# Kernel optimization log

Measured on AMD Instinct MI355X. Metric: run time of the kernel, lower is better.

## Reference

```python
import jax, jax.numpy as jnp
from jax import lax
import numpy as np

# Model hyper-parameters (from init_kwargs)
B = 4
POINT_NUM = 32768
SKP_NUM = 512
ISK_NUM = 2
K1 = 32                       # skp_neighbor_num
K2 = int(K1 * SKP_NUM * 4 / POINT_NUM)   # = 2, as computed in __init__
RADIUS_SCALING = 1.5
SPHERE_N = 128                # points per sphere template


def _fibonacci_sphere(n):
    i = np.arange(n, dtype=np.float64) + 0.5
    phi = np.arccos(1.0 - 2.0 * i / n)
    theta = np.pi * (1.0 + 5.0 ** 0.5) * i
    return np.stack([np.cos(theta) * np.sin(phi),
                     np.sin(theta) * np.sin(phi),
                     np.cos(phi)], axis=-1).astype(np.float32)


def setup_inputs() -> dict:
    key = jax.random.key(0)
    xyz = jax.random.normal(key, (B, POINT_NUM, 3), dtype=jnp.float32)
    sphere_template = jnp.asarray(_fibonacci_sphere(SPHERE_N))  # [S,3] unit sphere
    return {"xyz": xyz, "sphere_template": sphere_template}


def _fps(xyz, n):
    """Iterative furthest point sampling. xyz: [B,N,3] -> indices [B,n] int32."""
    b, N, _ = xyz.shape
    dist0 = jnp.full((b, N), 1e10, dtype=xyz.dtype)
    last0 = jnp.zeros((b,), dtype=jnp.int32)

    def step(carry, _):
        dist, last = carry
        lp = jnp.take_along_axis(xyz, last[:, None, None], axis=1)  # [B,1,3]
        d = jnp.sum((xyz - lp) ** 2, axis=-1)                        # [B,N]
        dist = jnp.minimum(dist, d)
        nxt = jnp.argmax(dist, axis=-1).astype(jnp.int32)
        return (dist, nxt), last

    (_, _), idxs = lax.scan(step, (dist0, last0), None, length=n)
    return idxs.T  # [B,n]


def _pairwise_sqdist(centers, pts):
    # [B,M,N] squared distances
    c2 = jnp.sum(centers ** 2, axis=-1)[:, :, None]
    p2 = jnp.sum(pts ** 2, axis=-1)[:, None, :]
    cp = jnp.einsum('bmd,bnd->bmn', centers, pts)
    return c2 + p2 - 2.0 * cp


def _sklnz(centers, pts, k):
    """SkeletonizationBlock: move each center to the mean of its k nearest
    points in pts; radius = mean distance to those neighbors."""
    d2 = _pairwise_sqdist(centers, pts)          # [B,M,N]
    neg, idx = lax.top_k(-d2, k)                 # [B,M,k]
    nb = jax.vmap(lambda x, i: x[i])(pts, idx)   # [B,M,k,3]
    new_centers = jnp.mean(nb, axis=2)
    radius = jnp.mean(jnp.sqrt(jnp.clip(-neg, 0.0)), axis=2)  # [B,M]
    return new_centers, radius


def _forward(xyz, sphere_template):
    # Stage 1: FPS to 4*skp_num seeds, then iterative skeletonization
    ids = _fps(xyz, SKP_NUM * 4)                               # [B,4*skp]
    centers = jnp.take_along_axis(xyz, ids[:, :, None], axis=1)
    radius = None
    for _ in range(ISK_NUM):
        centers, radius = _sklnz(centers, xyz, K1)
    # Stage 2: FPS on intermediate skeleton down to skp_num
    xyz2 = centers
    ids2 = _fps(xyz2, SKP_NUM)                                 # [B,skp]
    centers = jnp.take_along_axis(xyz2, ids2[:, :, None], axis=1)
    radius = jnp.take_along_axis(radius, ids2, axis=1)
    for _ in range(ISK_NUM):
        centers, _radius = _sklnz(centers, xyz2, K2)
    radius = (radius + _radius) * RADIUS_SCALING               # [B,skp]
    # Sphere reconstruction: template scaled by radius, translated to centers
    sphere_points = centers[:, :, None, :] + radius[:, :, None, None] * sphere_template[None, None]
    return centers, sphere_points, radius


def reference(xyz, sphere_template):
    return _forward(xyz, sphere_template)
```

## Files before the change

kernel.cpp:

```cpp
#include <hip/hip_runtime.h>
#include <cstdint>

#define BATCH 4
#define NPTS  32768
#define QN    8192
#define SKP   512
#define M1    (SKP*4)
#define KA    32
#define KB    2
#define SPHN  128

__device__ __forceinline__ float sqdist(float px, float py, float pz,
                                        float cx, float cy, float cz) {
  float dx = px - cx, dy = py - cy, dz = pz - cz;
  return __fadd_rn(__fadd_rn(__fmul_rn(dx, dx), __fmul_rn(dy, dy)),
                   __fmul_rn(dz, dz));
}
__device__ __forceinline__ float d2gram(float px, float py, float pz,
                                        float qx, float qy, float qz, float q2) {
  float p2 = __fadd_rn(__fadd_rn(__fmul_rn(px, px), __fmul_rn(py, py)),
                       __fmul_rn(pz, pz));
  float cp = __fadd_rn(__fadd_rn(__fmul_rn(qx, px), __fmul_rn(qy, py)),
                       __fmul_rn(qz, pz));
  return __fsub_rn(__fadd_rn(q2, p2), __fadd_rn(cp, cp));
}

__device__ __forceinline__ unsigned long long shfl_xor_u64(unsigned long long v, int off) {
  int lo = __shfl_xor((int)(unsigned)v, off);
  int hi = __shfl_xor((int)(unsigned)(v >> 32), off);
  return ((unsigned long long)(unsigned)hi << 32) | (unsigned)lo;
}
__device__ __forceinline__ unsigned long long shfl_u64(unsigned long long v, int src) {
  int lo = __shfl((int)(unsigned)v, src);
  int hi = __shfl((int)(unsigned)(v >> 32), src);
  return ((unsigned long long)(unsigned)hi << 32) | (unsigned)lo;
}

__global__ __launch_bounds__(1024)
void fps1_kernel(const float* __restrict__ xyz, int* __restrict__ ids,
                 unsigned long long* __restrict__ sync)
{
  int blk = blockIdx.x;
  int b = blk >> 2, sub = blk & 3;
  const float* X = xyz + (size_t)b * NPTS * 3;
  ids += (size_t)b * M1;
  int tid = threadIdx.x, lane = tid & 63, wave = tid >> 6;
  int base = sub * QN;

  __shared__ float2 xysh[QN];
  __shared__ unsigned long long s_w[16][2];
  __shared__ float s_pivc[16][3];
  __shared__ int s_J;

  float zr[8], dist[8];
#pragma unroll
  for (int j = 0; j < 8; ++j) {
    int pl = tid + 1024 * j;
    int pg = base + pl;
    xysh[pl] = make_float2(X[3*pg], X[3*pg+1]);
    zr[j] = X[3*pg+2];
    dist[j] = 1e10f;
  }
  if (tid == 0) {
    s_pivc[0][0] = X[0]; s_pivc[0][1] = X[1]; s_pivc[0][2] = X[2];
    if (sub == 0) ids[0] = 0;
  }
  __syncthreads();

  int it = 1, J = 1, rc = 1;

  while (it < M1) {
    for (int jp0 = 0; jp0 < J; jp0 += 4) {
      float pxa[4], pya[4], pza[4];
#pragma unroll
      for (int l = 0; l < 4; ++l) {
        int jj = jp0 + l; jj = (jj < J) ? jj : jp0;
        pxa[l] = s_pivc[jj][0]; pya[l] = s_pivc[jj][1]; pza[l] = s_pivc[jj][2];
      }
#pragma unroll
      for (int j = 0; j < 8; ++j) {
        int pl = tid + 1024 * j;
        float2 c2 = xysh[pl];
        float dd = dist[j];
#pragma unroll
        for (int l = 0; l < 4; ++l)
          dd = fminf(dd, sqdist(c2.x, c2.y, zr[j], pxa[l], pya[l], pza[l]));
        dist[j] = dd;
      }
    }
    unsigned long long k1 = 0, k2 = 0;
#pragma unroll
    for (int j = 0; j < 8; ++j) {
      int pg = base + tid + 1024 * j;
      unsigned long long key =
          ((unsigned long long)__float_as_uint(dist[j]) << 15) |
          (unsigned)(0x7FFF - pg);
      if (key > k1) { k2 = k1; k1 = key; }
      else if (key > k2) { k2 = key; }
    }
#pragma unroll
    for (int off = 32; off > 0; off >>= 1) {
      unsigned long long o1 = shfl_xor_u64(k1, off);
      unsigned long long o2 = shfl_xor_u64(k2, off);
      if (o1 > k1) { unsigned long long t = k1; k1 = o1; k2 = (t > o2) ? t : o2; }
      else         { k2 = (k2 > o1) ? k2 : o1; }
    }
    if (lane == 0) { s_w[wave][0] = k1; s_w[wave][1] = k2; }
    __syncthreads();
    if (wave == 0) {
      unsigned long long c1 = 0, c2v = 0;
      if (lane < 16) { c1 = s_w[lane][0]; c2v = s_w[lane][1]; }
      unsigned long long fb = c2v;
#pragma unroll
      for (int off = 8; off > 0; off >>= 1) {
        unsigned long long o = shfl_xor_u64(fb, off);
        if (o > fb) fb = o;
      }
      fb = shfl_u64(fb, 0);
      unsigned tag = (unsigned)rc;
      int par = rc & 1;
      int sbase = ((b * 2 + par) * 4 + sub) * 20;
      if (lane < 16)
        __hip_atomic_store(&sync[sbase + lane], (c1 << 12) | tag,
                           __ATOMIC_RELAXED, __HIP_MEMORY_SCOPE_AGENT);
      if (lane == 0)
        __hip_atomic_store(&sync[sbase + 16], (fb << 12) | tag,
                           __ATOMIC_RELAXED, __HIP_MEMORY_SCOPE_AGENT);
      unsigned long long ck = c1;
      unsigned long long rfk = 0;
      int cslot = 0, fslot = 0;
      bool needc = (lane >= 16), needf = (lane >= 1 && lane <= 3);
      if (needc) {
        int rsub = (sub + (lane >> 4)) & 3;
        cslot = ((b * 2 + par) * 4 + rsub) * 20 + (lane & 15);
      }
      if (needf) {
        int rsub = (sub + lane) & 3;
        fslot = ((b * 2 + par) * 4 + rsub) * 20 + 16;
      }
      while (__any(needc || needf)) {
        if (needc) {
          unsigned long long v = __hip_atomic_load(&sync[cslot],
                                  __ATOMIC_RELAXED, __HIP_MEMORY_SCOPE_AGENT);
          if ((unsigned)(v & 0xFFFu) == tag) { ck = v >> 12; needc = false; }
        }
        if (needf) {
          unsigned long long v = __hip_atomic_load(&sync[fslot],
                                  __ATOMIC_RELAXED, __HIP_MEMORY_SCOPE_AGENT);
          if ((unsigned)(v & 0xFFFu) == tag) { rfk = v >> 12; needf = false; }
        }
      }
      unsigned long long f = fb;
      unsigned long long f1 = shfl_u64(rfk, 1);
      unsigned long long f2 = shfl_u64(rfk, 2);
      unsigned long long f3 = shfl_u64(rfk, 3);
      if (f1 > f) f = f1;
      if (f2 > f) f = f2;
      if (f3 > f) f = f3;
      int ci = 0x7FFF - (int)(ck & 0x7FFFu);
      float cx = X[3*ci], cy = X[3*ci+1], cz = X[3*ci+2];
      int Jn = 0;
      while (it + Jn < M1 && Jn < 16) {
        unsigned long long mk = ck;
#pragma unroll
        for (int off = 32; off > 0; off >>= 1) {
          unsigned long long o = shfl_xor_u64(mk, off);
          if (o > mk) mk = o;
        }
        if (!(mk > f)) break;
        unsigned long long ball = __ballot(ck == mk);
        int wl = __ffsll(ball) - 1;
        float px = __shfl(cx, wl), py = __shfl(cy, wl), pz = __shfl(cz, wl);
        if (lane == 0) {
          s_pivc[Jn][0] = px; s_pivc[Jn][1] = py; s_pivc[Jn][2] = pz;
          if (sub == 0) ids[it + Jn] = 0x7FFF - (int)(mk & 0x7FFFu);
        }
        float d = sqdist(cx, cy, cz, px, py, pz);
        float nv = fminf(__uint_as_float((unsigned)(ck >> 15)), d);
        ck = ((unsigned long long)__float_as_uint(nv) << 15) | (ck & 0x7FFFu);
        ++Jn;
      }
      if (lane == 0) s_J = Jn;
    }
    __syncthreads();
    J = s_J;
    it += J;
    rc += 1;
  }
}

__global__ __launch_bounds__(256)
void fps2_kernel(const float4* __restrict__ pts, int* __restrict__ ids)
{
  const int PTS = 8, BLOCK = 256, NW = 4;
  int b = blockIdx.x;
  pts += (size_t)b * M1;
  ids += (size_t)b * SKP;
  int tid = threadIdx.x, lane = tid & 63, wave = tid >> 6;

  __shared__ float4 pl[M1];
  __shared__ float s_v[2][NW];
  __shared__ int   s_i[2][NW];

  float dist[PTS];
#pragma unroll
  for (int j = 0; j < PTS; ++j) {
    int p = tid + BLOCK * j;
    pl[p] = pts[p];
    dist[j] = 1e10f;
  }
  __syncthreads();

  if (tid == 0) ids[0] = 0;
  float4 piv = pl[0];
  float cx = piv.x, cy = piv.y, cz = piv.z;

  for (int it = 1; it < SKP; ++it) {
    float best = -1.f; int besti = 0;
#pragma unroll
    for (int j = 0; j < PTS; ++j) {
      int p = tid + BLOCK * j;
      float4 f = pl[p];
      float d = sqdist(f.x, f.y, f.z, cx, cy, cz);
      d = fminf(dist[j], d);
      dist[j] = d;
      bool gt = d > best;
      best  = gt ? d : best;
      besti = gt ? p : besti;
    }
#pragma unroll
    for (int off = 32; off > 0; off >>= 1) {
      float ov = __shfl_xor(best, off);
      int   oi = __shfl_xor(besti, off);
      if (ov > best || (ov == best && oi < besti)) { best = ov; besti = oi; }
    }
    int par = it & 1;
    if (lane == 0) { s_v[par][wave] = best; s_i[par][wave] = besti; }
    __syncthreads();
    float v = -1.f; int i = 0x7fffffff;
    if (lane < NW) { v = s_v[par][lane]; i = s_i[par][lane]; }
#pragma unroll
    for (int off = NW >> 1; off > 0; off >>= 1) {
      float ov = __shfl_xor(v, off);
      int   oi = __shfl_xor(i, off);
      if (ov > v || (ov == v && oi < i)) { v = ov; i = oi; }
    }
    i = __shfl(i, 0);
    if (tid == 0) ids[it] = i;
    float4 pv = pl[i];
    cx = pv.x; cy = pv.y; cz = pv.z;
  }
}

template<int K, int KL, int N, bool S3>
__global__ __launch_bounds__(256)
void sklnz_kernel(const float4* __restrict__ queries,
                  const void*   __restrict__ ptsv,
                  float4* __restrict__ outc,
                  float*  __restrict__ outr,
                  int M)
{
  const int CH = N / 64;
  int wave = threadIdx.x >> 6, lane = threadIdx.x & 63;
  int qid = blockIdx.x * 4 + wave;
  int b = qid / M;
  const float*  P3 = (const float*)ptsv + (size_t)b * N * 3;
  const float4* P4 = (const float4*)ptsv + (size_t)b * N;
  float4 q = queries[qid];
  float q2 = __fadd_rn(__fadd_rn(__fmul_rn(q.x, q.x), __fmul_rn(q.y, q.y)),
                       __fmul_rn(q.z, q.z));

  __shared__ float heads[4][64][K + 1];

  float a[KL];
#pragma unroll
  for (int s = 0; s < KL; ++s) a[s] = 3.0e38f;
  for (int j = 0; j < CH; ++j) {
    int p = lane + 64 * j;
    float px, py, pz;
    if (S3) { px = P3[3*p]; py = P3[3*p+1]; pz = P3[3*p+2]; }
    else    { float4 f = P4[p]; px = f.x; py = f.y; pz = f.z; }
    float d = d2gram(px, py, pz, q.x, q.y, q.z, q2);
#pragma unroll
    for (int s = KL - 1; s > 0; --s) a[s] = fminf(a[s], fmaxf(a[s-1], d));
    a[0] = fminf(a[0], d);
  }
#pragma unroll
  for (int s = 0; s < KL; ++s) heads[wave][lane][s] = a[s];
  heads[wave][lane][KL] = 3.1e38f;
  int h = 0; float t = 0.f;
  for (int r = 0; r < K; ++r) {
    float mv = heads[wave][lane][h];
    int   ml = lane;
#pragma unroll
    for (int off = 32; off > 0; off >>= 1) {
      float ov = __shfl_xor(mv, off);
      int   ol = __shfl_xor(ml, off);
      if (ov < mv || (ov == mv && ol < ml)) { mv = ov; ml = ol; }
    }
    t = mv;
    if (ml == lane) h++;
  }

  float sx = 0.f, sy = 0.f, sz = 0.f, sr = 0.f;
  int cl = 0;
  int myNext = 0x7fffffff;
  for (int j = 0; j < CH; ++j) {
    int p = lane + 64 * j;
    float px, py, pz;
    if (S3) { px = P3[3*p]; py = P3[3*p+1]; pz = P3[3*p+2]; }
    else    { float4 f = P4[p]; px = f.x; py = f.y; pz = f.z; }
    float d = d2gram(px, py, pz, q.x, q.y, q.z, q2);
    if (d < t) { sx += px; sy += py; sz += pz; sr += sqrtf(fmaxf(d, 0.f)); cl++; }
    else if (d == t && myNext == 0x7fffffff) myNext = p;
  }
  int ctot = cl;
#pragma unroll
  for (int off = 32; off > 0; off >>= 1) ctot += __shfl_xor(ctot, off);

  if constexpr (KL < K) {
    if (ctot >= K) {
      float a2[K];
#pragma unroll
      for (int s = 0; s < K; ++s) a2[s] = 3.0e38f;
      for (int j = 0; j < CH; ++j) {
        int p = lane + 64 * j;
        float px, py, pz;
        if (S3) { px = P3[3*p]; py = P3[3*p+1]; pz = P3[3*p+2]; }
        else    { float4 f = P4[p]; px = f.x; py = f.y; pz = f.z; }
        float d = d2gram(px, py, pz, q.x, q.y, q.z, q2);
#pragma unroll
        for (int s = K - 1; s > 0; --s) a2[s] = fminf(a2[s], fmaxf(a2[s-1], d));
        a2[0] = fminf(a2[0], d);
      }
#pragma unroll
      for (int s = 0; s < K; ++s) heads[wave][lane][s] = a2[s];
      heads[wave][lane][K] = 3.1e38f;
      h = 0;
      for (int r = 0; r < K; ++r) {
        float mv = heads[wave][lane][h];
        int   ml = lane;
#pragma unroll
        for (int off = 32; off > 0; off >>= 1) {
          float ov = __shfl_xor(mv, off);
          int   ol = __shfl_xor(ml, off);
          if (ov < mv || (ov == mv && ol < ml)) { mv = ov; ml = ol; }
        }
        t = mv;
        if (ml == lane) h++;
      }
      sx = sy = sz = sr = 0.f; cl = 0; myNext = 0x7fffffff;
      for (int j = 0; j < CH; ++j) {
        int p = lane + 64 * j;
        float px, py, pz;
        if (S3) { px = P3[3*p]; py = P3[3*p+1]; pz = P3[3*p+2]; }
        else    { float4 f = P4[p]; px = f.x; py = f.y; pz = f.z; }
        float d = d2gram(px, py, pz, q.x, q.y, q.z, q2);
        if (d < t) { sx += px; sy += py; sz += pz; sr += sqrtf(fmaxf(d, 0.f)); cl++; }
        else if (d == t && myNext == 0x7fffffff) myNext = p;
      }
      ctot = cl;
#pragma unroll
      for (int off = 32; off > 0; off >>= 1) ctot += __shfl_xor(ctot, off);
    }
  }

  int need = K - ctot;
  float rt = sqrtf(fmaxf(t, 0.f));

  for (int e = 0; e < need; ++e) {
    int mn = myNext;
#pragma unroll
    for (int off = 32; off > 0; off >>= 1) mn = min(mn, __shfl_xor(mn, off));
    if (myNext == mn) {
      float px, py, pz;
      if (S3) { px = P3[3*mn]; py = P3[3*mn+1]; pz = P3[3*mn+2]; }
      else    { float4 f = P4[mn]; px = f.x; py = f.y; pz = f.z; }
      sx += px; sy += py; sz += pz; sr += rt;
      int nx = 0x7fffffff;
      for (int j = (mn - lane) / 64 + 1; j < CH; ++j) {
        int p = lane + 64 * j;
        float ux, uy, uz;
        if (S3) { ux = P3[3*p]; uy = P3[3*p+1]; uz = P3[3*p+2]; }
        else    { float4 f = P4[p]; ux = f.x; uy = f.y; uz = f.z; }
        float d = d2gram(ux, uy, uz, q.x, q.y, q.z, q2);
        if (d == t) { nx = p; break; }
      }
      myNext = nx;
    }
  }

#pragma unroll
  for (int off = 32; off > 0; off >>= 1) {
    sx += __shfl_xor(sx, off);
    sy += __shfl_xor(sy, off);
    sz += __shfl_xor(sz, off);
    sr += __shfl_xor(sr, off);
  }
  if (lane == 0) {
    const float inv = 1.0f / (float)K;
    outc[qid] = make_float4(sx * inv, sy * inv, sz * inv, 0.f);
    outr[qid] = sr * inv;
  }
}

__global__ void gather1_kernel(const float* __restrict__ xyz,
                               const int* __restrict__ ids,
                               float4* __restrict__ cen)
{
  int g = blockIdx.x * 256 + threadIdx.x;
  if (g >= BATCH * M1) return;
  int b = g / M1;
  size_t base = ((size_t)b * NPTS + ids[g]) * 3;
  cen[g] = make_float4(xyz[base], xyz[base+1], xyz[base+2], 0.f);
}

__global__ void gather2_kernel(const float4* __restrict__ cen4,
                               const float* __restrict__ rad1,
                               const int* __restrict__ ids2,
                               float4* __restrict__ cen2,
                               float* __restrict__ radg)
{
  int g = blockIdx.x * 256 + threadIdx.x;
  if (g >= BATCH * SKP) return;
  int b = g / SKP;
  int p = ids2[g];
  cen2[g] = cen4[(size_t)b * M1 + p];
  radg[g] = rad1[(size_t)b * M1 + p];
}

__global__ void finalize_kernel(const float4* __restrict__ cen,
                                const float* __restrict__ radg,
                                const float* __restrict__ rad2,
                                const float* __restrict__ tmpl,
                                float* __restrict__ out)
{
  int g = blockIdx.x * 256 + threadIdx.x;
  int s = g >> 7;
  int j = g & 127;
  float4 c = cen[s];
  float r = __fmul_rn(__fadd_rn(radg[s], rad2[s]), 1.5f);
  float tx = tmpl[3*j], ty = tmpl[3*j+1], tz = tmpl[3*j+2];
  float* sp = out + BATCH * SKP * 3;
  sp[3*g]     = __fadd_rn(c.x, __fmul_rn(r, tx));
  sp[3*g + 1] = __fadd_rn(c.y, __fmul_rn(r, ty));
  sp[3*g + 2] = __fadd_rn(c.z, __fmul_rn(r, tz));
  if (j == 0) {
    out[3*s] = c.x; out[3*s+1] = c.y; out[3*s+2] = c.z;
    out[BATCH*SKP*3 + BATCH*SKP*SPHN*3 + s] = r;
  }
}

extern "C" void kernel_launch(void* const* d_in, const int* in_sizes, int n_in,
                              void* d_out, int out_size, void* d_ws, size_t ws_size,
                              hipStream_t stream)
{
  const float* xyz  = (const float*)d_in[0];
  const float* tmpl = (const float*)d_in[1];
  float* out = (float*)d_out;
  char* ws = (char*)d_ws;

  int*    ids1  = (int*)   (ws + 0);
  float4* cen4a = (float4*)(ws + 32768);
  float4* cen4b = (float4*)(ws + 163840);
  float*  rad1  = (float*) (ws + 294912);
  int*    ids2  = (int*)   (ws + 327680);
  float4* cen2a = (float4*)(ws + 335872);
  float4* cen2b = (float4*)(ws + 368640);
  float*  radg  = (float*) (ws + 401408);
  float*  rad2  = (float*) (ws + 409600);
  unsigned long long* sync = (unsigned long long*)(ws + 417792);

  fps1_kernel<<<BATCH * 4, 1024, 0, stream>>>(xyz, ids1, sync);
  gather1_kernel<<<(BATCH * M1 + 255) / 256, 256, 0, stream>>>(xyz, ids1, cen4a);
  sklnz_kernel<KA, 8, NPTS, true><<<BATCH * M1 / 4, 256, 0, stream>>>(cen4a, xyz, cen4b, rad1, M1);
  sklnz_kernel<KA, 8, NPTS, true><<<BATCH * M1 / 4, 256, 0, stream>>>(cen4b, xyz, cen4a, rad1, M1);
  fps2_kernel<<<BATCH, 256, 0, stream>>>(cen4a, ids2);
  gather2_kernel<<<(BATCH * SKP + 255) / 256, 256, 0, stream>>>(cen4a, rad1, ids2, cen2a, radg);
  sklnz_kernel<KB, KB, M1, false><<<BATCH * SKP / 4, 256, 0, stream>>>(cen2a, cen4a, cen2b, rad2, SKP);
  sklnz_kernel<KB, KB, M1, false><<<BATCH * SKP / 4, 256, 0, stream>>>(cen2b, cen4a, cen2a, rad2, SKP);
  finalize_kernel<<<BATCH * SKP * SPHN / 256, 256, 0, stream>>>(cen2a, radg, rad2, tmpl, out);
}
```

Measured before the change: 4.413 ms.

## Widen FPS speculative candidate pools to top-3 per wave and batch fps2 iterations

The multi-block FPS1 now tracks the top three keys per wave. It exchanges 32 candidates per sub-block plus a floor bound (the global max of each wave's third-best), so up to 32 FPS steps can be resolved per global synchronisation round instead of 16. FPS2 is rewritten from one-pivot-per-iteration with 256 threads to 1024 threads using the same speculative batched-pivot scheme, cutting the number of block-wide barriers. The cost is more shuffle and insertion work per round and more polling traffic on the sync slots.

After: 4.079 ms. 7.6% less time.

```diff
diff --git a/kernel.cpp b/kernel.cpp
--- a/kernel.cpp
+++ b/kernel.cpp
@@ -35,6 +35,18 @@
   int hi = __shfl((int)(unsigned)(v >> 32), src);
   return ((unsigned long long)(unsigned)hi << 32) | (unsigned)lo;
 }
+__device__ __forceinline__ unsigned long long umax64(unsigned long long a, unsigned long long b) {
+  return a > b ? a : b;
+}
+__device__ __forceinline__ unsigned long long umin64(unsigned long long a, unsigned long long b) {
+  return a < b ? a : b;
+}
+__device__ __forceinline__ void ins3(unsigned long long& k1, unsigned long long& k2,
+                                     unsigned long long& k3, unsigned long long v) {
+  k3 = umax64(k3, umin64(k2, v));
+  k2 = umax64(k2, umin64(k1, v));
+  k1 = umax64(k1, v);
+}
 
 __global__ __launch_bounds__(1024)
 void fps1_kernel(const float* __restrict__ xyz, int* __restrict__ ids,
@@ -48,8 +60,8 @@
   int base = sub * QN;
 
   __shared__ float2 xysh[QN];
-  __shared__ unsigned long long s_w[16][2];
-  __shared__ float s_pivc[16][3];
+  __shared__ unsigned long long s_w[16][3];
+  __shared__ float s_pivc[32][3];
   __shared__ int s_J;
 
   float zr[8], dist[8];
@@ -88,29 +100,28 @@
         dist[j] = dd;
       }
     }
-    unsigned long long k1 = 0, k2 = 0;
+    unsigned long long k1 = 0, k2 = 0, k3 = 0;
 #pragma unroll
     for (int j = 0; j < 8; ++j) {
       int pg = base + tid + 1024 * j;
       unsigned long long key =
           ((unsigned long long)__float_as_uint(dist[j]) << 15) |
           (unsigned)(0x7FFF - pg);
-      if (key > k1) { k2 = k1; k1 = key; }
-      else if (key > k2) { k2 = key; }
+      ins3(k1, k2, k3, key);
     }
 #pragma unroll
     for (int off = 32; off > 0; off >>= 1) {
       unsigned long long o1 = shfl_xor_u64(k1, off);
       unsigned long long o2 = shfl_xor_u64(k2, off);
-      if (o1 > k1) { unsigned long long t = k1; k1 = o1; k2 = (t > o2) ? t : o2; }
-      else         { k2 = (k2 > o1) ? k2 : o1; }
-    }
-    if (lane == 0) { s_w[wave][0] = k1; s_w[wave][1] = k2; }
+      unsigned long long o3 = shfl_xor_u64(k3, off);
+      ins3(k1, k2, k3, o1);
+      ins3(k1, k2, k3, o2);
+      ins3(k1, k2, k3, o3);
+    }
+    if (lane == 0) { s_w[wave][0] = k1; s_w[wave][1] = k2; s_w[wave][2] = k3; }
     __syncthreads();
     if (wave == 0) {
-      unsigned long long c1 = 0, c2v = 0;
-      if (lane < 16) { c1 = s_w[lane][0]; c2v = s_w[lane][1]; }
-      unsigned long long fb = c2v;
+      unsigned long long fb = (lane < 16) ? s_w[lane][2] : 0;
 #pragma unroll
       for (int off = 8; off > 0; off >>= 1) {
         unsigned long long o = shfl_xor_u64(fb, off);
@@ -119,65 +130,75 @@
       fb = shfl_u64(fb, 0);
       unsigned tag = (unsigned)rc;
       int par = rc & 1;
-      int sbase = ((b * 2 + par) * 4 + sub) * 20;
-      if (lane < 16)
-        __hip_atomic_store(&sync[sbase + lane], (c1 << 12) | tag,
+      int sbase = ((b * 2 + par) * 4 + sub) * 40;
+      unsigned long long mycand = 0;
+      if (lane < 16)      mycand = s_w[lane][0];
+      else if (lane < 32) mycand = s_w[lane - 16][1];
+      if (lane < 32)
+        __hip_atomic_store(&sync[sbase + lane], (mycand << 12) | tag,
                            __ATOMIC_RELAXED, __HIP_MEMORY_SCOPE_AGENT);
-      if (lane == 0)
-        __hip_atomic_store(&sync[sbase + 16], (fb << 12) | tag,
+      if (lane == 32)
+        __hip_atomic_store(&sync[sbase + 32], (fb << 12) | tag,
                            __ATOMIC_RELAXED, __HIP_MEMORY_SCOPE_AGENT);
-      unsigned long long ck = c1;
-      unsigned long long rfk = 0;
-      int cslot = 0, fslot = 0;
-      bool needc = (lane >= 16), needf = (lane >= 1 && lane <= 3);
-      if (needc) {
-        int rsub = (sub + (lane >> 4)) & 3;
-        cslot = ((b * 2 + par) * 4 + rsub) * 20 + (lane & 15);
-      }
-      if (needf) {
-        int rsub = (sub + lane) & 3;
-        fslot = ((b * 2 + par) * 4 + rsub) * 20 + 16;
-      }
-      while (__any(needc || needf)) {
-        if (needc) {
-          unsigned long long v = __hip_atomic_load(&sync[cslot],
+      int rel = (sub + (lane >> 4)) & 3;
+      int cb = ((b * 2 + par) * 4 + rel) * 40;
+      int c0s = cb + (lane & 15);
+      int c1s = cb + 16 + (lane & 15);
+      int fsl = ((b * 2 + par) * 4 + ((sub + lane) & 3)) * 40 + 32;
+      unsigned long long ck0 = 0, ck1 = 0, flr = 0;
+      bool n0 = true, n1 = true, nf = (lane < 4);
+      while (__any(n0 || n1 || nf)) {
+        if (n0) {
+          unsigned long long v = __hip_atomic_load(&sync[c0s],
                                   __ATOMIC_RELAXED, __HIP_MEMORY_SCOPE_AGENT);
-          if ((unsigned)(v & 0xFFFu) == tag) { ck = v >> 12; needc = false; }
-        }
-        if (needf) {
-          unsigned long long v = __hip_atomic_load(&sync[fslot],
+          if ((unsigned)(v & 0xFFFu) == tag) { ck0 = v >> 12; n0 = false; }
+        }
+        if (n1) {
+          unsigned long long v = __hip_atomic_load(&sync[c1s],
                                   __ATOMIC_RELAXED, __HIP_MEMORY_SCOPE_AGENT);
-          if ((unsigned)(v & 0xFFFu) == tag) { rfk = v >> 12; needf = false; }
-        }
-      }
-      unsigned long long f = fb;
-      unsigned long long f1 = shfl_u64(rfk, 1);
-      unsigned long long f2 = shfl_u64(rfk, 2);
-      unsigned long long f3 = shfl_u64(rfk, 3);
-      if (f1 > f) f = f1;
-      if (f2 > f) f = f2;
-      if (f3 > f) f = f3;
-      int ci = 0x7FFF - (int)(ck & 0x7FFFu);
-      float cx = X[3*ci], cy = X[3*ci+1], cz = X[3*ci+2];
+          if ((unsigned)(v & 0xFFFu) == tag) { ck1 = v >> 12; n1 = false; }
+        }
+        if (nf) {
+          unsigned long long v = __hip_atomic_load(&sync[fsl],
+                                  __ATOMIC_RELAXED, __HIP_MEMORY_SCOPE_AGENT);
+          if ((unsigned)(v & 0xFFFu) == tag) { flr = v >> 12; nf = false; }
+        }
+      }
+      unsigned long long f = umax64(umax64(shfl_u64(flr, 0), shfl_u64(flr, 1)),
+                                    umax64(shfl_u64(flr, 2), shfl_u64(flr, 3)));
+      int ci0 = 0x7FFF - (int)(ck0 & 0x7FFFu);
+      int ci1 = 0x7FFF - (int)(ck1 & 0x7FFFu);
+      float cx0 = X[3*ci0], cy0 = X[3*ci0+1], cz0 = X[3*ci0+2];
+      float cx1 = X[3*ci1], cy1 = X[3*ci1+1], cz1 = X[3*ci1+2];
       int Jn = 0;
-      while (it + Jn < M1 && Jn < 16) {
-        unsigned long long mk = ck;
+      while (it + Jn < M1 && Jn < 32) {
+        unsigned long long mk = umax64(ck0, ck1);
 #pragma unroll
         for (int off = 32; off > 0; off >>= 1) {
           unsigned long long o = shfl_xor_u64(mk, off);
           if (o > mk) mk = o;
         }
         if (!(mk > f)) break;
-        unsigned long long ball = __ballot(ck == mk);
-        int wl = __ffsll(ball) - 1;
-        float px = __shfl(cx, wl), py = __shfl(cy, wl), pz = __shfl(cz, wl);
+        unsigned long long b0 = __ballot(ck0 == mk);
+        float px, py, pz;
+        if (b0) {
+          int wl = __ffsll((long long)b0) - 1;
+          px = __shfl(cx0, wl); py = __shfl(cy0, wl); pz = __shfl(cz0, wl);
+        } else {
+          unsigned long long b1 = __ballot(ck1 == mk);
+          int wl = __ffsll((long long)b1) - 1;
+          px = __shfl(cx1, wl); py = __shfl(cy1, wl); pz = __shfl(cz1, wl);
+        }
         if (lane == 0) {
           s_pivc[Jn][0] = px; s_pivc[Jn][1] = py; s_pivc[Jn][2] = pz;
           if (sub == 0) ids[it + Jn] = 0x7FFF - (int)(mk & 0x7FFFu);
         }
-        float d = sqdist(cx, cy, cz, px, py, pz);
-        float nv = fminf(__uint_as_float((unsigned)(ck >> 15)), d);
-        ck = ((unsigned long long)__float_as_uint(nv) << 15) | (ck & 0x7FFFu);
+        float d0 = sqdist(cx0, cy0, cz0, px, py, pz);
+        float n0v = fminf(__uint_as_float((unsigned)(ck0 >> 15)), d0);
+        ck0 = ((unsigned long long)__float_as_uint(n0v) << 15) | (ck0 & 0x7FFFu);
+        float d1 = sqdist(cx1, cy1, cz1, px, py, pz);
+        float n1v = fminf(__uint_as_float((unsigned)(ck1 >> 15)), d1);
+        ck1 = ((unsigned long long)__float_as_uint(n1v) << 15) | (ck1 & 0x7FFFu);
         ++Jn;
       }
       if (lane == 0) s_J = Jn;
@@ -189,66 +210,101 @@
   }
 }
 
-__global__ __launch_bounds__(256)
+__global__ __launch_bounds__(1024)
 void fps2_kernel(const float4* __restrict__ pts, int* __restrict__ ids)
 {
-  const int PTS = 8, BLOCK = 256, NW = 4;
   int b = blockIdx.x;
   pts += (size_t)b * M1;
   ids += (size_t)b * SKP;
   int tid = threadIdx.x, lane = tid & 63, wave = tid >> 6;
 
   __shared__ float4 pl[M1];
-  __shared__ float s_v[2][NW];
-  __shared__ int   s_i[2][NW];
-
-  float dist[PTS];
-#pragma unroll
-  for (int j = 0; j < PTS; ++j) {
-    int p = tid + BLOCK * j;
-    pl[p] = pts[p];
-    dist[j] = 1e10f;
+  __shared__ unsigned long long s_w[16][3];
+  __shared__ float s_pivc[16][3];
+  __shared__ int s_J;
+
+  float4 f0 = pts[tid], f1 = pts[tid + 1024];
+  pl[tid] = f0; pl[tid + 1024] = f1;
+  float dist0 = 1e10f, dist1 = 1e10f;
+  if (tid == 0) {
+    ids[0] = 0;
+    s_pivc[0][0] = f0.x; s_pivc[0][1] = f0.y; s_pivc[0][2] = f0.z;
   }
   __syncthreads();
 
-  if (tid == 0) ids[0] = 0;
-  float4 piv = pl[0];
-  float cx = piv.x, cy = piv.y, cz = piv.z;
-
-  for (int it = 1; it < SKP; ++it) {
-    float best = -1.f; int besti = 0;
-#pragma unroll
-    for (int j = 0; j < PTS; ++j) {
-      int p = tid + BLOCK * j;
-      float4 f = pl[p];
-      float d = sqdist(f.x, f.y, f.z, cx, cy, cz);
-      d = fminf(dist[j], d);
-      dist[j] = d;
-      bool gt = d > best;
-      best  = gt ? d : best;
-      besti = gt ? p : besti;
+  int it = 1, J = 1;
+
+  while (it < SKP) {
+    for (int jp0 = 0; jp0 < J; jp0 += 4) {
+      float pxa[4], pya[4], pza[4];
+#pragma unroll
+      for (int l = 0; l < 4; ++l) {
+        int jj = jp0 + l; jj = (jj < J) ? jj : jp0;
+        pxa[l] = s_pivc[jj][0]; pya[l] = s_pivc[jj][1]; pza[l] = s_pivc[jj][2];
+      }
+#pragma unroll
+      for (int l = 0; l < 4; ++l) {
+        dist0 = fminf(dist0, sqdist(f0.x, f0.y, f0.z, pxa[l], pya[l], pza[l]));
+        dist1 = fminf(dist1, sqdist(f1.x, f1.y, f1.z, pxa[l], pya[l], pza[l]));
+      }
+    }
+    unsigned long long k1, k2 = 0, k3 = 0;
+    k1 = ((unsigned long long)__float_as_uint(dist0) << 15) | (unsigned)(0x7FFF - tid);
+    {
+      unsigned long long key =
+          ((unsigned long long)__float_as_uint(dist1) << 15) | (unsigned)(0x7FFF - (tid + 1024));
+      ins3(k1, k2, k3, key);
     }
 #pragma unroll
     for (int off = 32; off > 0; off >>= 1) {
-      float ov = __shfl_xor(best, off);
-      int   oi = __shfl_xor(besti, off);
-      if (ov > best || (ov == best && oi < besti)) { best = ov; besti = oi; }
-    }
-    int par = it & 1;
-    if (lane == 0) { s_v[par][wave] = best; s_i[par][wave] = besti; }
+      unsigned long long o1 = shfl_xor_u64(k1, off);
+      unsigned long long o2 = shfl_xor_u64(k2, off);
+      unsigned long long o3 = shfl_xor_u64(k3, off);
+      ins3(k1, k2, k3, o1);
+      ins3(k1, k2, k3, o2);
+      ins3(k1, k2, k3, o3);
+    }
+    if (lane == 0) { s_w[wave][0] = k1; s_w[wave][1] = k2; s_w[wave][2] = k3; }
     __syncthreads();
-    float v = -1.f; int i = 0x7fffffff;
-    if (lane < NW) { v = s_v[par][lane]; i = s_i[par][lane]; }
-#pragma unroll
-    for (int off = NW >> 1; off > 0; off >>= 1) {
-      float ov = __shfl_xor(v, off);
-      int   oi = __shfl_xor(i, off);
-      if (ov > v || (ov == v && oi < i)) { v = ov; i = oi; }
-    }
-    i = __shfl(i, 0);
-    if (tid == 0) ids[it] = i;
-    float4 pv = pl[i];
-    cx = pv.x; cy = pv.y; cz = pv.z;
+    if (wave == 0) {
+      unsigned long long fb = (lane < 16) ? s_w[lane][2] : 0;
+#pragma unroll
+      for (int off = 8; off > 0; off >>= 1) {
+        unsigned long long o = shfl_xor_u64(fb, off);
+        if (o > fb) fb = o;
+      }
+      unsigned long long f = shfl_u64(fb, 0);
+      unsigned long long ck = 0;
+      if (lane < 16)      ck = s_w[lane][0];
+      else if (lane < 32) ck = s_w[lane - 16][1];
+      int ci = (0x7FFF - (int)(ck & 0x7FFFu)) & (M1 - 1);
+      float4 c = pl[ci];
+      int Jn = 0;
+      while (it + Jn < SKP && Jn < 16) {
+        unsigned long long mk = ck;
+#pragma unroll
+        for (int off = 32; off > 0; off >>= 1) {
+          unsigned long long o = shfl_xor_u64(mk, off);
+          if (o > mk) mk = o;
+        }
+        if (!(mk > f)) break;
+        unsigned long long ball = __ballot(ck == mk);
+        int wl = __ffsll((long long)ball) - 1;
+        float px = __shfl(c.x, wl), py = __shfl(c.y, wl), pz = __shfl(c.z, wl);
+        if (lane == 0) {
+          s_pivc[Jn][0] = px; s_pivc[Jn][1] = py; s_pivc[Jn][2] = pz;
+          ids[it + Jn] = 0x7FFF - (int)(mk & 0x7FFFu);
+        }
+        float d = sqdist(c.x, c.y, c.z, px, py, pz);
+        float nv = fminf(__uint_as_float((unsigned)(ck >> 15)), d);
+        ck = ((unsigned long long)__float_as_uint(nv) << 15) | (ck & 0x7FFFu);
+        ++Jn;
+      }
+      if (lane == 0) s_J = Jn;
+    }
+    __syncthreads();
+    J = s_J;
+    it += J;
   }
 }
 
@@ -475,7 +531,7 @@
   gather1_kernel<<<(BATCH * M1 + 255) / 256, 256, 0, stream>>>(xyz, ids1, cen4a);
   sklnz_kernel<KA, 8, NPTS, true><<<BATCH * M1 / 4, 256, 0, stream>>>(cen4a, xyz, cen4b, rad1, M1);
   sklnz_kernel<KA, 8, NPTS, true><<<BATCH * M1 / 4, 256, 0, stream>>>(cen4b, xyz, cen4a, rad1, M1);
-  fps2_kernel<<<BATCH, 256, 0, stream>>>(cen4a, ids2);
+  fps2_kernel<<<BATCH, 1024, 0, stream>>>(cen4a, ids2);
   gather2_kernel<<<(BATCH * SKP + 255) / 256, 256, 0, stream>>>(cen4a, rad1, ids2, cen2a, radg);
   sklnz_kernel<KB, KB, M1, false><<<BATCH * SKP / 4, 256, 0, stream>>>(cen2a, cen4a, cen2b, rad2, SKP);
   sklnz_kernel<KB, KB, M1, false><<<BATCH * SKP / 4, 256, 0, stream>>>(cen2b, cen4a, cen2a, rad2, SKP);
```
